# Kernel tuning notes

Hardware: AMD Instinct MI355X
Metric: run time of the kernel (lower is better)

The kernel has to match this reference:

```python
import jax, jax.numpy as jnp
import numpy as np

C = 768            # config.channels
CH, CW = 16, 16    # coarse span shape for group 'screen'
N = CH * CW        # total coarse positions = 256
FH, FW, FP = 16, 16, 2
F = FH * FW * FP   # fine_total = 512
K = 4              # top4 sample mode
B = 1024           # sb


def _ln(x, g, b, eps=1e-5):
    m = jnp.mean(x, axis=-1, keepdims=True)
    v = jnp.mean((x - m) ** 2, axis=-1, keepdims=True)
    return (x - m) / jnp.sqrt(v + eps) * g + b


def _mlp3(x, W1, b1, W2, b2, W3, b3):
    h = jax.nn.gelu(x @ W1 + b1)
    h = jax.nn.gelu(h @ W2 + b2)
    return h @ W3 + b3


def setup_inputs() -> dict:
    key = jax.random.key(0)
    ks = jax.random.split(key, 16)

    def w(k, fan_in, shape):
        return jax.random.normal(k, shape, jnp.float32) * (1.0 / np.sqrt(fan_in))

    return {
        "x": jax.random.normal(ks[0], (B, C), jnp.float32),
        "g_in": jnp.ones((C,), jnp.float32),
        "b_in": jnp.zeros((C,), jnp.float32),
        # coarse head: C -> C -> C -> N
        "cW1": w(ks[1], C, (C, C)), "cb1": jnp.zeros((C,), jnp.float32),
        "cW2": w(ks[2], C, (C, C)), "cb2": jnp.zeros((C,), jnp.float32),
        "cW3": w(ks[3], C, (C, N)), "cb3": jnp.zeros((N,), jnp.float32),
        # coarse embedding
        "emb": jax.random.normal(ks[4], (N, C), jnp.float32),
        "g_e": jnp.ones((C,), jnp.float32),
        "b_e": jnp.zeros((C,), jnp.float32),
        # fine head: 2C -> C -> C -> F
        "fW1": w(ks[5], 2 * C, (2 * C, C)), "fb1": jnp.zeros((C,), jnp.float32),
        "fW2": w(ks[6], C, (C, C)), "fb2": jnp.zeros((C,), jnp.float32),
        "fW3": w(ks[7], C, (C, F)), "fb3": jnp.zeros((F,), jnp.float32),
        # no-op head
        "nW": w(ks[8], C, (C, 1)), "nb": jnp.zeros((1,), jnp.float32),
    }


def reference(x, g_in, b_in, cW1, cb1, cW2, cb2, cW3, cb3, emb, g_e, b_e,
              fW1, fb1, fW2, fb2, fW3, fb3, nW, nb):
    b = x.shape[0]
    xn = _ln(x, g_in, b_in)                                   # (b, C)
    no_op = xn @ nW + nb                                      # (b, 1)
    coarse = _mlp3(xn, cW1, cb1, cW2, cb2, cW3, cb3)          # (b, N)

    # top4 routing
    _, i = jax.lax.top_k(coarse, K)                           # (b, K) int32
    e = _ln(emb[i], g_e, b_e)                                 # (b, K, C)
    fine_in = jnp.concatenate(
        [jnp.broadcast_to(xn[:, None, :], (b, K, C)), e], axis=-1)  # (b, K, 2C)
    fine = _mlp3(fine_in, fW1, fb1, fW2, fb2, fW3, fb3)       # (b, K, F)

    log_f = jnp.log(jnp.float32(F))
    xfull = jnp.broadcast_to(coarse[:, :, None], (b, N, F)) - log_f  # (b, N, F)
    upd = fine + log_f - jax.nn.logsumexp(fine, axis=-1, keepdims=True)
    xfull = xfull.at[jnp.arange(b)[:, None], i].add(upd)      # scatter-combine

    # per-group permute: (b, ch, cw, fh, fw, fp) -> (b, ch, fh, cw, fw, fp)
    xg = xfull.reshape(b, CH, CW, FH, FW, FP)
    xg = jnp.transpose(xg, (0, 1, 3, 2, 4, 5)).reshape(b, -1)
    return jnp.concatenate([no_op, xg], axis=-1)              # (b, 1 + N*F)
```

## Files before the change

kernel.cpp:

```cpp
#include <hip/hip_runtime.h>
#include <hip/hip_bf16.h>
#include <math.h>

typedef unsigned short u16;
typedef unsigned int   u32;
typedef __attribute__((ext_vector_type(8))) short s16x8;
typedef __attribute__((ext_vector_type(4))) float f32x4;

#define CB 768
#define NB 256
#define FB 512
#define BATCH 1024
#define OUTC 131073
#define LOGF 6.2383246250395077f

__device__ __forceinline__ u16 f2bf(float f){
    u32 u = __float_as_uint(f);
    u32 r = u + 0x7FFFu + ((u >> 16) & 1u);
    return (u16)(r >> 16);
}
__device__ __forceinline__ float bf2f(u16 s){ return __uint_as_float(((u32)s) << 16); }
__device__ __forceinline__ bool probe_bf(const void* g){ return ((const u16*)g)[0] == 0x3F80u; }
__device__ __forceinline__ float loadraw(const void* p, size_t i, bool isbf){
    return isbf ? bf2f(((const u16*)p)[i]) : ((const float*)p)[i];
}
__device__ __forceinline__ void split3(float f, u16& h, u16& l, u16& q){
    h = f2bf(f); float r1 = f - bf2f(h);
    l = f2bf(r1); float r2 = r1 - bf2f(l);
    q = f2bf(r2);
}
__device__ __forceinline__ float gelu_f(float x){
    return 0.5f * x * (1.0f + tanhf(0.7978845608028654f * (x + 0.044715f * x * x * x)));
}
__device__ __forceinline__ f32x4 mfma16x16x32(s16x8 a, s16x8 b, f32x4 c){
    return __builtin_amdgcn_mfma_f32_16x16x32_bf16(a, b, c, 0, 0, 0);
}

__device__ __forceinline__ float blockReduce(float v, float* sb, bool domax){
    #pragma unroll
    for (int o = 32; o > 0; o >>= 1){
        float ov = __shfl_down(v, o, 64);
        v = domax ? fmaxf(v, ov) : (v + ov);
    }
    int w = threadIdx.x >> 6, lane = threadIdx.x & 63;
    if (lane == 0) sb[w] = v;
    __syncthreads();
    float r = domax ? fmaxf(fmaxf(sb[0], sb[1]), fmaxf(sb[2], sb[3]))
                    : (sb[0] + sb[1] + sb[2] + sb[3]);
    __syncthreads();
    return r;
}

struct TransDesc { const void* src; u16* dh; u16* dl; int K; int N; int start; int tilesX; };
struct TD6 { TransDesc d[6]; };

#define T_TRANS   3456
#define T_LNX_END 4480
#define T_LEM_END 4736
#define T_CI_END  4752
#define T_KS_END  4768
#define T_GRID    4769

__global__ __launch_bounds__(256) void prep_k(TD6 td,
        const void* x, const void* g, const void* bb, const void* nW, const void* nb,
        const void* emb, const void* ge, const void* be, const void* cb3, const void* ginp,
        u16* __restrict__ xh, u16* __restrict__ xl, u16* __restrict__ xq,
        u16* __restrict__ lnemb, float* __restrict__ noop,
        float* __restrict__ coarse, unsigned char* __restrict__ ksel,
        float* __restrict__ sumexp){
    __shared__ float t[32][33];
    __shared__ float sb[4];
    bool isbf = probe_bf(ginp);
    int blk = blockIdx.x, tid = threadIdx.x;
    if (blk < T_TRANS){
        int e = 0;
        #pragma unroll
        for (int i = 1; i < 6; i++) if (blk >= td.d[i].start) e = i;
        TransDesc d = td.d[e];
        int rel = blk - d.start;
        int n0 = (rel % d.tilesX) * 32;
        int k0 = (rel / d.tilesX) * 32;
        int tx = tid & 31, ty = tid >> 5;
        #pragma unroll
        for (int i = 0; i < 32; i += 8)
            t[ty + i][tx] = loadraw(d.src, (size_t)(k0 + ty + i) * d.N + n0 + tx, isbf);
        __syncthreads();
        #pragma unroll
        for (int i = 0; i < 32; i += 8){
            float f = t[tx][ty + i];
            u16 h = f2bf(f);
            d.dh[(size_t)(n0 + ty + i) * d.K + k0 + tx] = h;
            if (d.dl)
                d.dl[(size_t)(n0 + ty + i) * d.K + k0 + tx] = f2bf(f - bf2f(h));
        }
    } else if (blk < T_LNX_END){
        int b = blk - T_TRANS;
        float v[3];
        #pragma unroll
        for (int i = 0; i < 3; i++) v[i] = loadraw(x, (size_t)b * CB + tid + i * 256, isbf);
        float mean = blockReduce(v[0] + v[1] + v[2], sb, false) * (1.0f / 768.0f);
        float d0 = v[0] - mean, d1 = v[1] - mean, d2 = v[2] - mean;
        float var = blockReduce(d0*d0 + d1*d1 + d2*d2, sb, false) * (1.0f / 768.0f);
        float inv = 1.0f / sqrtf(var + 1e-5f);
        float dot = 0.0f;
        #pragma unroll
        for (int i = 0; i < 3; i++){
            int c = tid + i * 256;
            float xi = (v[i] - mean) * inv * loadraw(g, c, isbf) + loadraw(bb, c, isbf);
            u16 h, l, q; split3(xi, h, l, q);
            size_t o = (size_t)b * CB + c;
            xh[o] = h; xl[o] = l; xq[o] = q;
            dot += xi * loadraw(nW, c, isbf);
        }
        dot = blockReduce(dot, sb, false);
        if (tid == 0) noop[b] = dot + loadraw(nb, 0, isbf);
    } else if (blk < T_LEM_END){
        int n = blk - T_LNX_END;
        float v[3];
        #pragma unroll
        for (int i = 0; i < 3; i++) v[i] = loadraw(emb, (size_t)n * CB + tid + i * 256, isbf);
        float mean = blockReduce(v[0] + v[1] + v[2], sb, false) * (1.0f / 768.0f);
        float d0 = v[0] - mean, d1 = v[1] - mean, d2 = v[2] - mean;
        float var = blockReduce(d0*d0 + d1*d1 + d2*d2, sb, false) * (1.0f / 768.0f);
        float inv = 1.0f / sqrtf(var + 1e-5f);
        #pragma unroll
        for (int i = 0; i < 3; i++){
            int c = tid + i * 256;
            lnemb[(size_t)n * CB + c] =
                f2bf((v[i] - mean) * inv * loadraw(ge, c, isbf) + loadraw(be, c, isbf));
        }
    } else if (blk < T_CI_END){
        int base = (blk - T_LEM_END) * 16384;
        #pragma unroll
        for (int j = 0; j < 64; j++){
            int i = base + j * 256 + tid;
            coarse[i] = loadraw(cb3, i & 255, isbf);
        }
    } else if (blk < T_KS_END){
        int base = (blk - T_CI_END) * 4096;
        u32* kp = (u32*)ksel;
        #pragma unroll
        for (int j = 0; j < 16; j++) kp[base + j * 256 + tid] = 0xFFFFFFFFu;
    } else {
        #pragma unroll
        for (int j = 0; j < 16; j++) sumexp[j * 256 + tid] = 0.0f;
    }
}

template<int ASPLIT, int BSPLIT, int ACT, int OUTMODE, int TM, int TN, int GATHER>
__device__ __forceinline__ void gemm_body(u16* sm,
        const u16* __restrict__ Ah, const u16* __restrict__ Al, const u16* __restrict__ Aq,
        const int* __restrict__ gidx,
        const u16* __restrict__ Bth, const u16* __restrict__ Btl,
        const void* __restrict__ bias, bool isbf,
        void* __restrict__ o0, void* __restrict__ o1, void* __restrict__ o2,
        int bx, int by, int kbeg, int kend, int N, int lda, int ldb){
    constexpr int LDA = 72;
    constexpr int MT = TM / 32;
    constexpr int NT = TN / 64;
    constexpr int AC = TM / 64;
    constexpr int BC = TN / 64;
    u16* As = sm;
    u16* Bs = sm + ASPLIT * TM * LDA;
    const int m0 = by * TM, n0 = bx * TN;
    const int tid = threadIdx.x;
    const int w = tid >> 6, lane = tid & 63, lm = lane & 15, q = lane >> 4;
    const int wr = w & 1, wc = w >> 1;
    f32x4 acc[MT][NT];
    #pragma unroll
    for (int i = 0; i < MT; i++)
        #pragma unroll
        for (int j = 0; j < NT; j++) acc[i][j] = (f32x4)(0.0f);
    const int ar = (AC == 2) ? (tid >> 2) : (tid >> 3);
    const int ac = (AC == 2) ? ((tid & 3) * 16) : ((tid & 7) * 8);
    const int bn = (BC == 2) ? (tid >> 2) : (tid >> 3);
    const int bc = (BC == 2) ? ((tid & 3) * 16) : ((tid & 7) * 8);
    const u16* Apl[3] = { Ah, Al, Aq };
    const u16* Bpl[2] = { Bth, Btl };
    const int arow = GATHER ? gidx[m0 + ar] : (m0 + ar);

    s16x8 pa[ASPLIT][AC], pb[BSPLIT][BC];
    auto load_regs = [&](int kk){
        #pragma unroll
        for (int s = 0; s < ASPLIT; s++){
            const u16* sp = Apl[s] + (size_t)arow * lda + kk + ac;
            pa[s][0] = *(const s16x8*)(sp);
            if (AC == 2) pa[s][1] = *(const s16x8*)(sp + 8);
        }
        #pragma unroll
        for (int s = 0; s < BSPLIT; s++){
            const u16* sp = Bpl[s] + (size_t)(n0 + bn) * ldb + kk + bc;
            pb[s][0] = *(const s16x8*)(sp);
            if (BC == 2) pb[s][1] = *(const s16x8*)(sp + 8);
        }
    };

    load_regs(kbeg);
    for (int k0 = kbeg; k0 < kend; k0 += 64){
        __syncthreads();
        #pragma unroll
        for (int s = 0; s < ASPLIT; s++){
            *(s16x8*)&As[s*TM*LDA + ar*LDA + ac] = pa[s][0];
            if (AC == 2) *(s16x8*)&As[s*TM*LDA + ar*LDA + ac + 8] = pa[s][1];
        }
        #pragma unroll
        for (int s = 0; s < BSPLIT; s++){
            *(s16x8*)&Bs[s*TN*LDA + bn*LDA + bc] = pb[s][0];
            if (BC == 2) *(s16x8*)&Bs[s*TN*LDA + bn*LDA + bc + 8] = pb[s][1];
        }
        __syncthreads();
        if (k0 + 64 < kend) load_regs(k0 + 64);

        #pragma unroll
        for (int kk = 0; kk < 2; kk++){
            s16x8 afr[ASPLIT][MT], bfr[BSPLIT][NT];
            #pragma unroll
            for (int mt = 0; mt < MT; mt++)
                #pragma unroll
                for (int s = 0; s < ASPLIT; s++)
                    afr[s][mt] = *(const s16x8*)&As[s*TM*LDA + ((mt*2 + wr)*16 + lm)*LDA + kk*32 + q*8];
            #pragma unroll
            for (int nt = 0; nt < NT; nt++)
                #pragma unroll
                for (int s = 0; s < BSPLIT; s++)
                    bfr[s][nt] = *(const s16x8*)&Bs[s*TN*LDA + ((nt*4 + wc)*16 + lm)*LDA + kk*32 + q*8];
            #pragma unroll
            for (int mt = 0; mt < MT; mt++)
                #pragma unroll
                for (int nt = 0; nt < NT; nt++){
                    acc[mt][nt] = mfma16x16x32(afr[0][mt], bfr[0][nt], acc[mt][nt]);
                    if (ASPLIT == 3){
                        acc[mt][nt] = mfma16x16x32(afr[1][mt], bfr[0][nt], acc[mt][nt]);
                        acc[mt][nt] = mfma16x16x32(afr[2][mt], bfr[0][nt], acc[mt][nt]);
                    }
                    if (BSPLIT == 2){
                        acc[mt][nt] = mfma16x16x32(afr[0][mt], bfr[1][nt], acc[mt][nt]);
                        if (ASPLIT == 3)
                            acc[mt][nt] = mfma16x16x32(afr[1][mt], bfr[1][nt], acc[mt][nt]);
                    }
                }
        }
    }

    if (OUTMODE == 3){
        #pragma unroll
        for (int nt = 0; nt < NT; nt++){
            int n = n0 + (nt*4 + wc)*16 + lm;
            #pragma unroll
            for (int mt = 0; mt < MT; mt++)
                #pragma unroll
                for (int r = 0; r < 4; r++){
                    int m = m0 + (mt*2 + wr)*16 + q*4 + r;
                    atomicAdd(&((float*)o0)[(size_t)m * N + n], acc[mt][nt][r]);
                }
        }
    } else if (OUTMODE == 4){
        #pragma unroll
        for (int mt = 0; mt < MT; mt++)
            #pragma unroll
            for (int r = 0; r < 4; r++){
                int m = m0 + (mt*2 + wr)*16 + q*4 + r;
                float esum = 0.0f;
                #pragma unroll
                for (int nt = 0; nt < NT; nt++){
                    int n = n0 + (nt*4 + wc)*16 + lm;
                    float vv = acc[mt][nt][r] + (bias ? loadraw(bias, n, isbf) : 0.0f);
                    ((float*)o0)[(size_t)m * N + n] = vv;
                    esum += expf(vv);
                }
                #pragma unroll
                for (int o = 8; o > 0; o >>= 1) esum += __shfl_down(esum, o, 16);
                if (lm == 0) atomicAdd(&((float*)o1)[m], esum);
            }
    } else if (OUTMODE == 5){
        #pragma unroll
        for (int nt = 0; nt < NT; nt++){
            int n = n0 + (nt*4 + wc)*16 + lm;
            float bv = bias ? loadraw(bias, n, isbf) : 0.0f;
            #pragma unroll
            for (int mt = 0; mt < MT; mt++){
                #pragma unroll
                for (int r = 0; r < 4; r++){
                    int m = m0 + (mt*2 + wr)*16 + q*4 + r;
                    float xv = ((const float*)o1)[(size_t)(m >> 2) * N + n];
                    ((u16*)o0)[(size_t)m * N + n] = f2bf(gelu_f(acc[mt][nt][r] + bv + xv));
                }
            }
        }
    } else {
        #pragma unroll
        for (int nt = 0; nt < NT; nt++){
            int n = n0 + (nt*4 + wc)*16 + lm;
            float bv = bias ? loadraw(bias, n, isbf) : 0.0f;
            #pragma unroll
            for (int mt = 0; mt < MT; mt++){
                #pragma unroll
                for (int r = 0; r < 4; r++){
                    int m = m0 + (mt*2 + wr)*16 + q*4 + r;
                    float vv = acc[mt][nt][r] + bv;
                    if (ACT == 1) vv = gelu_f(vv);
                    size_t o = (size_t)m * N + n;
                    if (OUTMODE == 0)      ((float*)o0)[o] = vv;
                    else if (OUTMODE == 1) ((u16*)o0)[o] = f2bf(vv);
                    else {
                        u16 h, l, qq; split3(vv, h, l, qq);
                        ((u16*)o0)[o] = h; ((u16*)o1)[o] = l; ((u16*)o2)[o] = qq;
                    }
                }
            }
        }
    }
}

template<int ASPLIT, int BSPLIT, int ACT, int OUTMODE, int TM, int TN, int GATHER, int MINW>
__global__ __launch_bounds__(512, MINW) void gemm_k(
        const u16* __restrict__ Ah, const u16* __restrict__ Al, const u16* __restrict__ Aq,
        const int* __restrict__ gidx,
        const u16* __restrict__ Bth, const u16* __restrict__ Btl,
        const void* __restrict__ bias, const void* __restrict__ ginp,
        void* __restrict__ o0, void* __restrict__ o1, void* __restrict__ o2,
        int K, int N, int lda, int ldb){
    __shared__ u16 sm[(ASPLIT * TM + BSPLIT * TN) * 72];
    bool isbf = probe_bf(ginp);
    const int kc = K / gridDim.z;
    const int kbeg = blockIdx.z * kc;
    gemm_body<ASPLIT, BSPLIT, ACT, OUTMODE, TM, TN, GATHER>(sm,
        Ah, Al, Aq, gidx, Bth, Btl, bias, isbf, o0, o1, o2,
        blockIdx.x, blockIdx.y, kbeg, kbeg + kc, N, lda, ldb);
}

__global__ __launch_bounds__(512, 2) void c1x_k(
        const u16* __restrict__ xh, const u16* __restrict__ xl, const u16* __restrict__ xq,
        const u16* __restrict__ cW1th, const u16* __restrict__ cW1tl,
        const void* __restrict__ cb1, const void* __restrict__ ginp,
        u16* __restrict__ h1h, u16* __restrict__ h1l, u16* __restrict__ h1q,
        const u16* __restrict__ fW1t, float* __restrict__ xpart,
        const u16* __restrict__ lnemb, float* __restrict__ embW){
    __shared__ u16 sm[(3 * 64 + 2 * 64) * 72];
    bool isbf = probe_bf(ginp);
    if (blockIdx.x < 192){
        gemm_body<3, 2, 1, 2, 64, 64, 0>(sm, xh, xl, xq, nullptr, cW1th, cW1tl,
            cb1, isbf, h1h, h1l, h1q, blockIdx.x % 12, blockIdx.x / 12, 0, 768,
            768, 768, 768);
    } else if (blockIdx.x < 240){
        int rel = blockIdx.x - 192;
        gemm_body<1, 1, 0, 0, 128, 128, 0>(sm, xh, nullptr, nullptr, nullptr, fW1t, nullptr,
            nullptr, isbf, xpart, nullptr, nullptr, rel % 6, rel / 6, 0, 768,
            768, 768, 1536);
    } else {
        int rel = blockIdx.x - 240;
        gemm_body<1, 1, 0, 0, 128, 128, 0>(sm, lnemb, nullptr, nullptr, nullptr, fW1t + 768, nullptr,
            nullptr, isbf, embW, nullptr, nullptr, rel % 6, rel / 6, 0, 768,
            768, 768, 1536);
    }
}

__global__ __launch_bounds__(512) void topk_fadd_k(const float* __restrict__ coarse,
        unsigned char* __restrict__ ksel,
        const float* __restrict__ embW, const float* __restrict__ xpart,
        const void* __restrict__ fb1, const void* __restrict__ ginp,
        u16* __restrict__ gg1){
    __shared__ int idx_s[32];
    int w = threadIdx.x >> 6, lane = threadIdx.x & 63;
    int b = blockIdx.x * 8 + w;
    const float* cr = coarse + (size_t)b * NB;
    float v[4]; int id[4];
    #pragma unroll
    for (int j = 0; j < 4; j++){ id[j] = lane + 64*j; v[j] = cr[id[j]]; }
    for (int k = 0; k < 4; k++){
        float bv = v[0]; int bi = id[0];
        #pragma unroll
        for (int j = 1; j < 4; j++)
            if (v[j] > bv || (v[j] == bv && id[j] < bi)){ bv = v[j]; bi = id[j]; }
        #pragma unroll
        for (int o = 32; o > 0; o >>= 1){
            float ov = __shfl_xor(bv, o, 64);
            int   oi = __shfl_xor(bi, o, 64);
            if (ov > bv || (ov == bv && oi < bi)){ bv = ov; bi = oi; }
        }
        if (lane == 0){
            idx_s[w*4 + k] = bi;
            ksel[(size_t)b * NB + bi] = (unsigned char)k;
        }
        #pragma unroll
        for (int j = 0; j < 4; j++) if (id[j] == bi) v[j] = -INFINITY;
    }
    __syncthreads();
    bool isbf = probe_bf(ginp);
    int fr0 = blockIdx.x * 32;
    #pragma unroll
    for (int j = 0; j < 6; j++){
        int c = (int)threadIdx.x + j * 512;
        int r = c / 96;
        int col = (c - r * 96) * 8;
        int fr = fr0 + r;
        int bb2 = fr >> 2;
        int n = idx_s[r];
        const float* ew = embW + (size_t)n * CB + col;
        const float* xr = xpart + (size_t)bb2 * CB + col;
        float4 e0 = *(const float4*)ew, e1 = *(const float4*)(ew + 4);
        float4 x0 = *(const float4*)xr, x1 = *(const float4*)(xr + 4);
        float ev[8] = {e0.x,e0.y,e0.z,e0.w,e1.x,e1.y,e1.z,e1.w};
        float xv[8] = {x0.x,x0.y,x0.z,x0.w,x1.x,x1.y,x1.z,x1.w};
        u16 res[8];
        #pragma unroll
        for (int e = 0; e < 8; e++){
            float bv = loadraw(fb1, col + e, isbf);
            res[e] = f2bf(gelu_f((ev[e] + bv) + xv[e]));
        }
        *(s16x8*)(gg1 + (size_t)fr * CB + col) = *(s16x8*)res;
    }
}

__global__ __launch_bounds__(256) void out_k(const float* __restrict__ coarse,
        const float* __restrict__ fine, const float* __restrict__ sumexp,
        const unsigned char* __restrict__ ksel, const float* __restrict__ noop,
        const void* __restrict__ ginp, void* __restrict__ outp){
    u32 g0 = ((u32)blockIdx.x * 256u + (u32)threadIdx.x) * 8u;
    const u32 total = (u32)BATCH * (u32)OUTC;
    if (g0 >= total) return;
    bool isbf = probe_bf(ginp);
    u32 qq = g0 >> 17;
    int rr = (int)(g0 & 131071u) - (int)qq;
    if (rr < 0){ qq -= 1u; rr += 131073; }
    int b = (int)qq;
    int lastkey = -1, ks = 255, fr = 0;
    float cv = 0.0f, lbase = 0.0f;
    float vals[8];
    #pragma unroll
    for (int e = 0; e < 8; e++){
        float val;
        if (rr == 0){
            val = noop[b];
        } else {
            int j = rr - 1;
            int n = ((j >> 13) << 4) | ((j >> 5) & 15);
            int key = (b << 8) | n;
            if (key != lastkey){
                lastkey = key;
                size_t o = (size_t)b * NB + n;
                cv = coarse[o] - LOGF;
                ks = ksel[o];
                if (ks != 255){
                    fr = b * 4 + ks;
                    lbase = LOGF - logf(sumexp[fr]);
                }
            }
            val = cv;
            if (ks != 255)
                val += fine[((size_t)fr << 9) + (((j >> 9) & 15) << 5) + (j & 31)] + lbase;
        }
        vals[e] = val;
        rr++;
        if (rr == 131073){ rr = 0; b++; }
    }
    if (isbf){
        u16 res[8];
        #pragma unroll
        for (int e = 0; e < 8; e++) res[e] = f2bf(vals[e]);
        *(s16x8*)((u16*)outp + g0) = *(s16x8*)res;
    } else {
        float* of = (float*)outp + g0;
        *(float4*)(of)     = make_float4(vals[0], vals[1], vals[2], vals[3]);
        *(float4*)(of + 4) = make_float4(vals[4], vals[5], vals[6], vals[7]);
    }
}

extern "C" void kernel_launch(void* const* d_in, const int* in_sizes, int n_in,
                              void* d_out, int out_size, void* d_ws, size_t ws_size,
                              hipStream_t stream){
    (void)in_sizes; (void)n_in; (void)out_size; (void)ws_size;
    char* ws = (char*)d_ws;
    size_t off = 0;
    auto alloc = [&](size_t bytes){ void* p = ws + off; off += (bytes + 255) & ~(size_t)255; return p; };

    u16* xh  = (u16*)alloc((size_t)1024*768*2);
    u16* xl  = (u16*)alloc((size_t)1024*768*2);
    u16* xq  = (u16*)alloc((size_t)1024*768*2);
    u16* h1h = (u16*)alloc((size_t)1024*768*2);
    u16* h1l = (u16*)alloc((size_t)1024*768*2);
    u16* h1q = (u16*)alloc((size_t)1024*768*2);
    u16* h2h = (u16*)alloc((size_t)1024*768*2);
    u16* h2l = (u16*)alloc((size_t)1024*768*2);
    u16* h2q = (u16*)alloc((size_t)1024*768*2);
    u16* lnemb = (u16*)alloc((size_t)256*768*2);
    float* coarse = (float*)alloc((size_t)1024*256*4);
    unsigned char* ksel = (unsigned char*)alloc((size_t)1024*256);
    float* noop   = (float*)alloc((size_t)1024*4);
    float* sumexp = (float*)alloc((size_t)4096*4);
    float* embW   = (float*)alloc((size_t)256*768*4);
    float* xpart  = (float*)alloc((size_t)1024*768*4);
    u16*   gg1    = (u16*)  alloc((size_t)4096*768*2);
    u16*   gg2    = (u16*)  alloc((size_t)4096*768*2);
    float* fine   = (float*)alloc((size_t)4096*512*4);
    u16* cW1th = (u16*)alloc((size_t)768*768*2);
    u16* cW1tl = (u16*)alloc((size_t)768*768*2);
    u16* cW2th = (u16*)alloc((size_t)768*768*2);
    u16* cW2tl = (u16*)alloc((size_t)768*768*2);
    u16* cW3th = (u16*)alloc((size_t)768*256*2);
    u16* cW3tl = (u16*)alloc((size_t)768*256*2);
    u16* fW1t  = (u16*)alloc((size_t)768*1536*2);
    u16* fW2t  = (u16*)alloc((size_t)768*768*2);
    u16* fW3t  = (u16*)alloc((size_t)512*768*2);

    const void* ginp = d_in[1];

    TD6 td;
    td.d[0] = { d_in[3],  cW1th, cW1tl,  768, 768,    0, 24 };
    td.d[1] = { d_in[5],  cW2th, cW2tl,  768, 768,  576, 24 };
    td.d[2] = { d_in[7],  cW3th, cW3tl,  768, 256, 1152,  8 };
    td.d[3] = { d_in[12], fW1t,  nullptr,1536, 768, 1344, 24 };
    td.d[4] = { d_in[14], fW2t,  nullptr, 768, 768, 2496, 24 };
    td.d[5] = { d_in[16], fW3t,  nullptr, 768, 512, 3072, 16 };

    prep_k<<<T_GRID, 256, 0, stream>>>(td, d_in[0], d_in[1], d_in[2], d_in[18], d_in[19],
            d_in[9], d_in[10], d_in[11], d_in[8], ginp,
            xh, xl, xq, lnemb, noop, coarse, ksel, sumexp);

    c1x_k<<<dim3(252, 1, 1), 512, 0, stream>>>(
            xh, xl, xq, cW1th, cW1tl, d_in[4], ginp, h1h, h1l, h1q,
            fW1t, xpart, lnemb, embW);

    gemm_k<3,2,1,2,64,64,0,2><<<dim3(12, 16, 1), 512, 0, stream>>>(
            h1h, h1l, h1q, nullptr, cW2th, cW2tl,
            d_in[6], ginp, h2h, h2l, h2q, 768, 768, 768, 768);
    gemm_k<3,2,0,3,64,64,0,2><<<dim3(4, 16, 4), 512, 0, stream>>>(
            h2h, h2l, h2q, nullptr, cW3th, cW3tl,
            nullptr, ginp, coarse, nullptr, nullptr, 768, 256, 768, 768);

    topk_fadd_k<<<128, 512, 0, stream>>>(coarse, ksel, embW, xpart, d_in[13], ginp, gg1);

    gemm_k<1,1,1,1,64,128,0,4><<<dim3(6, 64, 1), 512, 0, stream>>>(
            gg1, nullptr, nullptr, nullptr, fW2t, nullptr,
            d_in[15], ginp, gg2, nullptr, nullptr, 768, 768, 768, 768);
    gemm_k<1,1,0,4,64,128,0,4><<<dim3(4, 64, 1), 512, 0, stream>>>(
            gg2, nullptr, nullptr, nullptr, fW3t, nullptr,
            d_in[17], ginp, fine, sumexp, nullptr, 768, 512, 768, 768);

    u32 total_chunks = ((u32)BATCH * (u32)OUTC) / 8u;
    u32 blocks = (total_chunks + 255u) / 256u;
    out_k<<<blocks, 256, 0, stream>>>(coarse, fine, sumexp, ksel, noop, ginp, d_out);
}
```

Before: 714.9 us.

## Overlap bulk coarse-only output writes with fine-head GEMMs, then patch selected spans

The large output pass is split in two. The chunks that depend only on coarse values (non-selected spans) are written by extra blocks launched alongside the fine W2 and W3 GEMMs, so the memory-bound broadcast overlaps compute. A small follow-up kernel uses the saved top-k indices to write only the selected spans and the chunks that hold the no-op column or cross row boundaries. This adds idx storage and more complex kernels, and the writer blocks may compete with the GEMM blocks for CUs.

```diff
diff --git a/kernel.cpp b/kernel.cpp
--- a/kernel.cpp
+++ b/kernel.cpp
@@ -272,21 +272,6 @@
                 for (int o = 8; o > 0; o >>= 1) esum += __shfl_down(esum, o, 16);
                 if (lm == 0) atomicAdd(&((float*)o1)[m], esum);
             }
-    } else if (OUTMODE == 5){
-        #pragma unroll
-        for (int nt = 0; nt < NT; nt++){
-            int n = n0 + (nt*4 + wc)*16 + lm;
-            float bv = bias ? loadraw(bias, n, isbf) : 0.0f;
-            #pragma unroll
-            for (int mt = 0; mt < MT; mt++){
-                #pragma unroll
-                for (int r = 0; r < 4; r++){
-                    int m = m0 + (mt*2 + wr)*16 + q*4 + r;
-                    float xv = ((const float*)o1)[(size_t)(m >> 2) * N + n];
-                    ((u16*)o0)[(size_t)m * N + n] = f2bf(gelu_f(acc[mt][nt][r] + bv + xv));
-                }
-            }
-        }
     } else {
         #pragma unroll
         for (int nt = 0; nt < NT; nt++){
@@ -327,6 +312,125 @@
     gemm_body<ASPLIT, BSPLIT, ACT, OUTMODE, TM, TN, GATHER>(sm,
         Ah, Al, Aq, gidx, Bth, Btl, bias, isbf, o0, o1, o2,
         blockIdx.x, blockIdx.y, kbeg, kbeg + kc, N, lda, ldb);
+}
+
+__device__ __forceinline__ void out1_body(const float* __restrict__ coarse,
+        const unsigned char* __restrict__ ksel, bool isbf, void* __restrict__ outp,
+        u32 ch0, u32 ch1, u32 wtid, u32 stride){
+    for (u32 chn = ch0 + wtid; chn < ch1; chn += stride){
+        u32 g0 = chn * 8u;
+        u32 qq = g0 >> 17;
+        int rr = (int)(g0 & 131071u) - (int)qq;
+        if (rr < 0){ qq -= 1u; rr += 131073; }
+        int b = (int)qq;
+        if (rr == 0 || rr >= 131066) continue;
+        int lastn = -1; float cv = 0.0f; bool defer = false;
+        float vals[8];
+        #pragma unroll
+        for (int e = 0; e < 8; e++){
+            int j = rr - 1 + e;
+            int n = ((j >> 13) << 4) | ((j >> 5) & 15);
+            if (n != lastn){
+                lastn = n;
+                size_t o = (size_t)b * NB + n;
+                cv = coarse[o] - LOGF;
+                if (ksel[o] != 255) defer = true;
+            }
+            vals[e] = cv;
+        }
+        if (defer) continue;
+        if (isbf){
+            u16 res[8];
+            #pragma unroll
+            for (int e = 0; e < 8; e++) res[e] = f2bf(vals[e]);
+            *(s16x8*)((u16*)outp + g0) = *(s16x8*)res;
+        } else {
+            float* of = (float*)outp + g0;
+            *(float4*)(of)     = make_float4(vals[0], vals[1], vals[2], vals[3]);
+            *(float4*)(of + 4) = make_float4(vals[4], vals[5], vals[6], vals[7]);
+        }
+    }
+}
+
+template<int ASPLIT, int BSPLIT, int ACT, int OUTMODE, int TM, int TN, int MINW>
+__global__ __launch_bounds__(512, MINW) void gemm_out1_k(
+        const u16* __restrict__ Ah, const u16* __restrict__ Bth,
+        const void* __restrict__ bias, const void* __restrict__ ginp,
+        void* __restrict__ o0, void* __restrict__ o1,
+        int K, int N, int lda, int ldb, int gemmBlocks, int gx,
+        const float* __restrict__ coarse, const unsigned char* __restrict__ ksel,
+        void* __restrict__ outp, u32 ch0, u32 ch1){
+    __shared__ u16 sm[(ASPLIT * TM + BSPLIT * TN) * 72];
+    bool isbf = probe_bf(ginp);
+    int blk = blockIdx.x;
+    if (blk < gemmBlocks){
+        gemm_body<ASPLIT, BSPLIT, ACT, OUTMODE, TM, TN, 0>(sm,
+            Ah, nullptr, nullptr, nullptr, Bth, nullptr, bias, isbf,
+            o0, o1, nullptr, blk % gx, blk / gx, 0, K, N, lda, ldb);
+    } else {
+        u32 wblk = (u32)(blk - gemmBlocks);
+        u32 nwb  = (u32)(gridDim.x - gemmBlocks);
+        out1_body(coarse, ksel, isbf, outp, ch0, ch1,
+                  wblk * 512u + (u32)threadIdx.x, nwb * 512u);
+    }
+}
+
+__global__ __launch_bounds__(512) void topk_fadd_k(const float* __restrict__ coarse,
+        unsigned char* __restrict__ ksel, int* __restrict__ idxg,
+        const float* __restrict__ embW, const float* __restrict__ xpart,
+        const void* __restrict__ fb1, const void* __restrict__ ginp,
+        u16* __restrict__ gg1){
+    __shared__ int idx_s[32];
+    int w = threadIdx.x >> 6, lane = threadIdx.x & 63;
+    int b = blockIdx.x * 8 + w;
+    const float* cr = coarse + (size_t)b * NB;
+    float v[4]; int id[4];
+    #pragma unroll
+    for (int j = 0; j < 4; j++){ id[j] = lane + 64*j; v[j] = cr[id[j]]; }
+    for (int k = 0; k < 4; k++){
+        float bv = v[0]; int bi = id[0];
+        #pragma unroll
+        for (int j = 1; j < 4; j++)
+            if (v[j] > bv || (v[j] == bv && id[j] < bi)){ bv = v[j]; bi = id[j]; }
+        #pragma unroll
+        for (int o = 32; o > 0; o >>= 1){
+            float ov = __shfl_xor(bv, o, 64);
+            int   oi = __shfl_xor(bi, o, 64);
+            if (ov > bv || (ov == bv && oi < bi)){ bv = ov; bi = oi; }
+        }
+        if (lane == 0){
+            idx_s[w*4 + k] = bi;
+            idxg[b*4 + k] = bi;
+            ksel[(size_t)b * NB + bi] = (unsigned char)k;
+        }
+        #pragma unroll
+        for (int j = 0; j < 4; j++) if (id[j] == bi) v[j] = -INFINITY;
+    }
+    __syncthreads();
+    bool isbf = probe_bf(ginp);
+    int fr0 = blockIdx.x * 32;
+    #pragma unroll
+    for (int j = 0; j < 6; j++){
+        int c = (int)threadIdx.x + j * 512;
+        int r = c / 96;
+        int col = (c - r * 96) * 8;
+        int fr = fr0 + r;
+        int bb2 = fr >> 2;
+        int n = idx_s[r];
+        const float* ew = embW + (size_t)n * CB + col;
+        const float* xr = xpart + (size_t)bb2 * CB + col;
+        float4 e0 = *(const float4*)ew, e1 = *(const float4*)(ew + 4);
+        float4 x0 = *(const float4*)xr, x1 = *(const float4*)(xr + 4);
+        float ev[8] = {e0.x,e0.y,e0.z,e0.w,e1.x,e1.y,e1.z,e1.w};
+        float xv[8] = {x0.x,x0.y,x0.z,x0.w,x1.x,x1.y,x1.z,x1.w};
+        u16 res[8];
+        #pragma unroll
+        for (int e = 0; e < 8; e++){
+            float bv = loadraw(fb1, col + e, isbf);
+            res[e] = f2bf(gelu_f((ev[e] + bv) + xv[e]));
+        }
+        *(s16x8*)(gg1 + (size_t)fr * CB + col) = *(s16x8*)res;
+    }
 }
 
 __global__ __launch_bounds__(512, 2) void c1x_k(
@@ -355,71 +459,10 @@
     }
 }
 
-__global__ __launch_bounds__(512) void topk_fadd_k(const float* __restrict__ coarse,
-        unsigned char* __restrict__ ksel,
-        const float* __restrict__ embW, const float* __restrict__ xpart,
-        const void* __restrict__ fb1, const void* __restrict__ ginp,
-        u16* __restrict__ gg1){
-    __shared__ int idx_s[32];
-    int w = threadIdx.x >> 6, lane = threadIdx.x & 63;
-    int b = blockIdx.x * 8 + w;
-    const float* cr = coarse + (size_t)b * NB;
-    float v[4]; int id[4];
-    #pragma unroll
-    for (int j = 0; j < 4; j++){ id[j] = lane + 64*j; v[j] = cr[id[j]]; }
-    for (int k = 0; k < 4; k++){
-        float bv = v[0]; int bi = id[0];
-        #pragma unroll
-        for (int j = 1; j < 4; j++)
-            if (v[j] > bv || (v[j] == bv && id[j] < bi)){ bv = v[j]; bi = id[j]; }
-        #pragma unroll
-        for (int o = 32; o > 0; o >>= 1){
-            float ov = __shfl_xor(bv, o, 64);
-            int   oi = __shfl_xor(bi, o, 64);
-            if (ov > bv || (ov == bv && oi < bi)){ bv = ov; bi = oi; }
-        }
-        if (lane == 0){
-            idx_s[w*4 + k] = bi;
-            ksel[(size_t)b * NB + bi] = (unsigned char)k;
-        }
-        #pragma unroll
-        for (int j = 0; j < 4; j++) if (id[j] == bi) v[j] = -INFINITY;
-    }
-    __syncthreads();
-    bool isbf = probe_bf(ginp);
-    int fr0 = blockIdx.x * 32;
-    #pragma unroll
-    for (int j = 0; j < 6; j++){
-        int c = (int)threadIdx.x + j * 512;
-        int r = c / 96;
-        int col = (c - r * 96) * 8;
-        int fr = fr0 + r;
-        int bb2 = fr >> 2;
-        int n = idx_s[r];
-        const float* ew = embW + (size_t)n * CB + col;
-        const float* xr = xpart + (size_t)bb2 * CB + col;
-        float4 e0 = *(const float4*)ew, e1 = *(const float4*)(ew + 4);
-        float4 x0 = *(const float4*)xr, x1 = *(const float4*)(xr + 4);
-        float ev[8] = {e0.x,e0.y,e0.z,e0.w,e1.x,e1.y,e1.z,e1.w};
-        float xv[8] = {x0.x,x0.y,x0.z,x0.w,x1.x,x1.y,x1.z,x1.w};
-        u16 res[8];
-        #pragma unroll
-        for (int e = 0; e < 8; e++){
-            float bv = loadraw(fb1, col + e, isbf);
-            res[e] = f2bf(gelu_f((ev[e] + bv) + xv[e]));
-        }
-        *(s16x8*)(gg1 + (size_t)fr * CB + col) = *(s16x8*)res;
-    }
-}
-
-__global__ __launch_bounds__(256) void out_k(const float* __restrict__ coarse,
+__device__ __forceinline__ void out_chunk_general(u32 g0, const float* __restrict__ coarse,
         const float* __restrict__ fine, const float* __restrict__ sumexp,
         const unsigned char* __restrict__ ksel, const float* __restrict__ noop,
-        const void* __restrict__ ginp, void* __restrict__ outp){
-    u32 g0 = ((u32)blockIdx.x * 256u + (u32)threadIdx.x) * 8u;
-    const u32 total = (u32)BATCH * (u32)OUTC;
-    if (g0 >= total) return;
-    bool isbf = probe_bf(ginp);
+        bool isbf, void* __restrict__ outp){
     u32 qq = g0 >> 17;
     int rr = (int)(g0 & 131071u) - (int)qq;
     if (rr < 0){ qq -= 1u; rr += 131073; }
@@ -466,6 +509,35 @@
     }
 }
 
+__global__ __launch_bounds__(256) void out2_k(const float* __restrict__ coarse,
+        const float* __restrict__ fine, const float* __restrict__ sumexp,
+        const unsigned char* __restrict__ ksel, const int* __restrict__ idx,
+        const float* __restrict__ noop, const void* __restrict__ ginp,
+        void* __restrict__ outp){
+    bool isbf = probe_bf(ginp);
+    if (blockIdx.x == 1024){
+        #pragma unroll
+        for (int s = 0; s < 4; s++){
+            u32 b = (u32)threadIdx.x * 4u + (u32)s;
+            u32 g0 = (b * (u32)OUTC) & ~7u;
+            out_chunk_general(g0, coarse, fine, sumexp, ksel, noop, isbf, outp);
+        }
+        return;
+    }
+    int w = threadIdx.x >> 6, lane = threadIdx.x & 63;
+    int u = blockIdx.x * 4 + w;
+    int b = u >> 2;
+    int n = idx[u];
+    size_t base = (size_t)b * OUTC + 1 + ((size_t)(n >> 4) << 13) + ((size_t)(n & 15) << 5);
+    for (int t = lane; t < 16 * 5; t += 64){
+        int fh = t / 5, i = t % 5;
+        size_t gs = base + ((size_t)fh << 9);
+        u32 c = (u32)(gs >> 3) + (u32)i;
+        if ((size_t)c * 8u < gs + 32u)
+            out_chunk_general(c * 8u, coarse, fine, sumexp, ksel, noop, isbf, outp);
+    }
+}
+
 extern "C" void kernel_launch(void* const* d_in, const int* in_sizes, int n_in,
                               void* d_out, int out_size, void* d_ws, size_t ws_size,
                               hipStream_t stream){
@@ -488,6 +560,7 @@
     unsigned char* ksel = (unsigned char*)alloc((size_t)1024*256);
     float* noop   = (float*)alloc((size_t)1024*4);
     float* sumexp = (float*)alloc((size_t)4096*4);
+    int*   idx    = (int*)alloc((size_t)4096*4);
     float* embW   = (float*)alloc((size_t)256*768*4);
     float* xpart  = (float*)alloc((size_t)1024*768*4);
     u16*   gg1    = (u16*)  alloc((size_t)4096*768*2);
@@ -528,16 +601,17 @@
             h2h, h2l, h2q, nullptr, cW3th, cW3tl,
             nullptr, ginp, coarse, nullptr, nullptr, 768, 256, 768, 768);
 
-    topk_fadd_k<<<128, 512, 0, stream>>>(coarse, ksel, embW, xpart, d_in[13], ginp, gg1);
-
-    gemm_k<1,1,1,1,64,128,0,4><<<dim3(6, 64, 1), 512, 0, stream>>>(
-            gg1, nullptr, nullptr, nullptr, fW2t, nullptr,
-            d_in[15], ginp, gg2, nullptr, nullptr, 768, 768, 768, 768);
-    gemm_k<1,1,0,4,64,128,0,4><<<dim3(4, 64, 1), 512, 0, stream>>>(
-            gg2, nullptr, nullptr, nullptr, fW3t, nullptr,
-            d_in[17], ginp, fine, sumexp, nullptr, 768, 512, 768, 768);
-
-    u32 total_chunks = ((u32)BATCH * (u32)OUTC) / 8u;
-    u32 blocks = (total_chunks + 255u) / 256u;
-    out_k<<<blocks, 256, 0, stream>>>(coarse, fine, sumexp, ksel, noop, ginp, d_out);
-}
+    topk_fadd_k<<<128, 512, 0, stream>>>(coarse, ksel, idx, embW, xpart, d_in[13], ginp, gg1);
+
+    const u32 TOTCH = ((u32)BATCH * (u32)OUTC) / 8u;
+    const u32 HALF  = TOTCH / 2u;
+
+    gemm_out1_k<1,1,1,1,64,128,4><<<dim3(384 + 768, 1, 1), 512, 0, stream>>>(
+            gg1, fW2t, d_in[15], ginp, gg2, nullptr,
+            768, 768, 768, 768, 384, 6, coarse, ksel, d_out, 0u, HALF);
+    gemm_out1_k<1,1,0,4,64,128,4><<<dim3(256 + 768, 1, 1), 512, 0, stream>>>(
+            gg2, fW3t, d_in[17], ginp, fine, sumexp,
+            768, 512, 768, 768, 256, 4, coarse, ksel, d_out, HALF, TOTCH);
+
+    out2_k<<<1025, 256, 0, stream>>>(coarse, fine, sumexp, ksel, idx, noop, ginp, d_out);
+}
```

Measured after the change: 729.6 us. 1.02x slower.
